# Kernel optimization log

Hardware: AMD Instinct MI355X
Metric: run time of the kernel (lower is better)

The kernel has to match this reference:

```python
import jax, jax.numpy as jnp
import numpy as np

B, S, D, H = 4, 2048, 1024, 16
HD = D // H  # head_dim = 64


def setup_inputs() -> dict:
    key = jax.random.key(0)
    ks = jax.random.split(key, 8)
    scale = 1.0 / np.sqrt(D)
    return {
        "hidden_states": jax.random.normal(ks[0], (B, S, D), dtype=jnp.float32),
        "attention_mask": jnp.zeros((B, 1, 1, S), dtype=jnp.float32),
        "Wq": jax.random.normal(ks[1], (D, D), dtype=jnp.float32) * scale,
        "bq": jnp.zeros((D,), dtype=jnp.float32),
        "Wk": jax.random.normal(ks[2], (D, D), dtype=jnp.float32) * scale,
        "bk": jnp.zeros((D,), dtype=jnp.float32),
        "Wv": jax.random.normal(ks[3], (D, D), dtype=jnp.float32) * scale,
        "bv": jnp.zeros((D,), dtype=jnp.float32),
    }


def reference(hidden_states, attention_mask, Wq, bq, Wk, bk, Wv, bv):
    def split_heads(x):
        # [B,S,D] -> [B,H,S,HD]
        return x.reshape(B, S, H, HD).transpose(0, 2, 1, 3)

    q = split_heads(hidden_states @ Wq + bq)
    k = split_heads(hidden_states @ Wk + bk)
    v = split_heads(hidden_states @ Wv + bv)

    # [B,H,S,S]
    scores = jnp.einsum("bhqd,bhkd->bhqk", q, k) / jnp.sqrt(jnp.float32(HD))
    scores = scores + attention_mask  # additive mask, broadcasts [B,1,1,S]
    probs = jax.nn.softmax(scores, axis=-1)

    ctx = jnp.einsum("bhqk,bhkd->bhqd", probs, v)  # [B,H,S,HD]
    return ctx.transpose(0, 2, 1, 3).reshape(B, S, D)
```

## Files before the change

kernel.cpp:

```cpp
#include <hip/hip_runtime.h>
#include <hip/hip_bf16.h>
#include <stdint.h>

typedef __attribute__((ext_vector_type(4))) float f32x4;
typedef __attribute__((ext_vector_type(16))) float f32x16;
typedef __attribute__((ext_vector_type(8))) short bf16x8;
typedef __attribute__((ext_vector_type(4))) int int4v;
typedef __attribute__((ext_vector_type(8))) unsigned short u16x8;
typedef unsigned int u32;

static __device__ __forceinline__ unsigned short f2bf(float f) {
    union { float f; unsigned u; } v; v.f = f;
    unsigned r = v.u + 0x7FFF + ((v.u >> 16) & 1);
    return (unsigned short)(r >> 16);
}

static __device__ __forceinline__ u32 cvtpk(float lo, float hi) {
    u32 r;
    asm("v_cvt_pk_bf16_f32 %0, %1, %2" : "=v"(r) : "v"(lo), "v"(hi));
    return r;
}

static __device__ __forceinline__ void pl32swap_u(u32& a, u32& b) {
    asm("v_permlane32_swap_b32 %0, %1" : "+v"(a), "+v"(b));
}

__global__ __launch_bounds__(256) void cvt_x_kernel(const float* __restrict__ x,
                                                    unsigned short* __restrict__ xb) {
    int i = (blockIdx.x * 256 + threadIdx.x) * 4;
    float4 v = *(const float4*)(x + i);
    ushort4 o = make_ushort4(f2bf(v.x), f2bf(v.y), f2bf(v.z), f2bf(v.w));
    *(ushort4*)(xb + i) = o;
}

__global__ __launch_bounds__(256) void cvt_w_kernel(const float* __restrict__ Wq,
                                                    const float* __restrict__ Wk,
                                                    const float* __restrict__ Wv,
                                                    unsigned short* __restrict__ Wt3) {
    const float* W = (blockIdx.z == 0) ? Wq : ((blockIdx.z == 1) ? Wk : Wv);
    unsigned short* out = Wt3 + (size_t)blockIdx.z * 1024 * 1024;
    __shared__ unsigned short t[64][68];
    int k0 = blockIdx.x * 64, n0 = blockIdx.y * 64;
    int tid = threadIdx.x;
#pragma unroll
    for (int i = 0; i < 4; i++) {
        int c = i * 256 + tid;
        int row = c >> 4, cb = c & 15;
        float4 v = *(const float4*)(W + (size_t)(k0 + row) * 1024 + n0 + cb * 4);
        ushort4 o = make_ushort4(f2bf(v.x), f2bf(v.y), f2bf(v.z), f2bf(v.w));
        *(ushort4*)(&t[row][cb * 4]) = o;
    }
    __syncthreads();
#pragma unroll
    for (int i = 0; i < 2; i++) {
        int c = i * 256 + tid;
        int n = c >> 3, kc = c & 7;
        u16x8 tmp;
#pragma unroll
        for (int j = 0; j < 8; j++) tmp[j] = t[kc * 8 + j][n];
        *(u16x8*)(&out[(size_t)(n0 + n) * 1024 + k0 + kc * 8]) = tmp;
    }
}

__global__ __launch_bounds__(256) void mask_reorder_kernel(const float* __restrict__ mask,
                                                           float* __restrict__ maskr) {
    int o = blockIdx.x * 256 + threadIdx.x;
    int reg = o & 15, kvb = (o >> 4) & 1, hi2 = (o >> 5) & 1, kt = (o >> 6) & 31, bb = o >> 11;
    int kv = kt * 64 + kvb * 32 + (reg & 3) + 8 * (reg >> 2) + 4 * hi2;
    maskr[o] = 8.0f * mask[bb * 2048 + kv];
}

__global__ __launch_bounds__(256) void qkv_gemm_kernel(
    const unsigned short* __restrict__ Xb,
    const unsigned short* __restrict__ Wt3,
    const float* __restrict__ bq, const float* __restrict__ bk, const float* __restrict__ bv,
    unsigned short* __restrict__ Qo, unsigned short* __restrict__ Ko,
    unsigned short* __restrict__ Vt)
{
    int z = blockIdx.z;
    const unsigned short* Wt = Wt3 + (size_t)z * 1048576;
    const float* bias = (z == 0) ? bq : ((z == 1) ? bk : bv);
    int m0 = blockIdx.x * 128, n0 = blockIdx.y * 128;

    __shared__ unsigned short As[128 * 64];
    __shared__ unsigned short Bs[128 * 64];

    int tid = threadIdx.x, lane = tid & 63, wave = tid >> 6;
    int wm = wave >> 1, wn = wave & 1;
    int lr = lane & 15, lg = lane >> 4;
    int swzf = (lr & 7) << 4;

    f32x4 acc[4][4] = {};

    for (int kt = 0; kt < 16; kt++) {
        int kbase = kt * 64;
#pragma unroll
        for (int i = 0; i < 4; i++) {
            int c = i * 256 + tid;
            int row = c >> 3, cb = c & 7;
            int4v av = *(const int4v*)(Xb + (size_t)(m0 + row) * 1024 + kbase + cb * 8);
            int4v bv2 = *(const int4v*)(Wt + (size_t)(n0 + row) * 1024 + kbase + cb * 8);
            int off = row * 128 + ((cb * 16) ^ ((row & 7) << 4));
            *(int4v*)((char*)As + off) = av;
            *(int4v*)((char*)Bs + off) = bv2;
        }
        __syncthreads();
#pragma unroll
        for (int kk = 0; kk < 2; kk++) {
            bf16x8 a[4], bb[4];
#pragma unroll
            for (int mi = 0; mi < 4; mi++)
                a[mi] = *(const bf16x8*)((char*)As + (wm * 64 + mi * 16 + lr) * 128
                                         + ((kk * 64 + lg * 16) ^ swzf));
#pragma unroll
            for (int ni = 0; ni < 4; ni++)
                bb[ni] = *(const bf16x8*)((char*)Bs + (wn * 64 + ni * 16 + lr) * 128
                                          + ((kk * 64 + lg * 16) ^ swzf));
#pragma unroll
            for (int mi = 0; mi < 4; mi++)
#pragma unroll
                for (int ni = 0; ni < 4; ni++)
                    acc[mi][ni] = __builtin_amdgcn_mfma_f32_16x16x32_bf16(a[mi], bb[ni], acc[mi][ni], 0, 0, 0);
        }
        __syncthreads();
    }

    if (z < 2) {
        unsigned short* out = (z == 0) ? Qo : Ko;
#pragma unroll
        for (int ni = 0; ni < 4; ni++) {
            int n = n0 + wn * 64 + ni * 16 + lr;
            float bsv = bias[n];
#pragma unroll
            for (int mi = 0; mi < 4; mi++) {
                int mrow = m0 + wm * 64 + mi * 16 + lg * 4;
#pragma unroll
                for (int r = 0; r < 4; r++)
                    out[(size_t)(mrow + r) * 1024 + n] = f2bf(acc[mi][ni][r] + bsv);
            }
        }
    } else {
#pragma unroll
        for (int ni = 0; ni < 4; ni++) {
            int n = n0 + wn * 64 + ni * 16 + lr;
            float bsv = bias[n];
            int h = n >> 6, hd = n & 63;
#pragma unroll
            for (int mi = 0; mi < 4; mi++) {
                int mrow = m0 + wm * 64 + mi * 16 + lg * 4;
                int b = mrow >> 11, s = mrow & 2047;
                ushort4 pk = make_ushort4(f2bf(acc[mi][ni][0] + bsv),
                                          f2bf(acc[mi][ni][1] + bsv),
                                          f2bf(acc[mi][ni][2] + bsv),
                                          f2bf(acc[mi][ni][3] + bsv));
                *(ushort4*)(&Vt[((size_t)(b * 16 + h) * 64 + hd) * 2048 + s]) = pk;
            }
        }
    }
}

__global__ __launch_bounds__(256) void attn_kernel(
    const unsigned short* __restrict__ Q,
    const unsigned short* __restrict__ K,
    const unsigned short* __restrict__ Vt,
    const float* __restrict__ maskr,
    float* __restrict__ out)
{
    __shared__ __align__(16) char smem[33280];
    const int tid = threadIdx.x, lane = tid & 63, w = tid >> 6;
    const int ln31 = lane & 31, hi = lane >> 5;
    const int bh = blockIdx.y, b = bh >> 4, h = bh & 15;
    const int q0 = blockIdx.x * 128 + w * 32;
    const int swz = (ln31 & 7) << 4;
    const float c1 = 0.18033688011112042f;
    const float DTHR = 44.361f;

    const unsigned short* Qrow = Q + (size_t)(b * 2048 + q0 + ln31) * 1024 + h * 64;
    bf16x8 aq[4];
#pragma unroll
    for (int ds = 0; ds < 4; ds++) aq[ds] = *(const bf16x8*)(Qrow + ds * 16 + hi * 8);

    const unsigned short* Kbp = K + (size_t)b * 2048 * 1024 + h * 64;
    const unsigned short* Vbp = Vt + (size_t)bh * 64 * 2048;

    const int r0 = tid >> 3, cb = tid & 7;
    const int woff = r0 * 128 + ((cb * 16) ^ ((r0 & 7) << 4));

    const unsigned short* kp = Kbp + (size_t)r0 * 1024 + cb * 8;
    const unsigned short* vp = Vbp + (size_t)r0 * 2048 + cb * 8;
    const float* mp = maskr + (size_t)b * 2048 + tid * 4;

    f32x16 oacc0 = {}, oacc1 = {};
    float mrun = -1e30f, lrun = 0.f;

    int4v kr0, kr1, vr0, vr1, mr = {};
    kr0 = *(const int4v*)kp; kr1 = *(const int4v*)(kp + 32 * 1024);
    vr0 = *(const int4v*)vp; vr1 = *(const int4v*)(vp + 32 * 2048);
    if (tid < 16) mr = *(const int4v*)mp;
    kp += 65536; vp += 64; mp += 64;
    *(int4v*)(smem + woff) = kr0;
    *(int4v*)(smem + 32 * 128 + woff) = kr1;
    *(int4v*)(smem + 16384 + woff) = vr0;
    *(int4v*)(smem + 16384 + 32 * 128 + woff) = vr1;
    if (tid < 16) *(int4v*)(smem + 32768 + tid * 16) = mr;
    kr0 = *(const int4v*)kp; kr1 = *(const int4v*)(kp + 32 * 1024);
    vr0 = *(const int4v*)vp; vr1 = *(const int4v*)(vp + 32 * 2048);
    if (tid < 16) mr = *(const int4v*)mp;
    kp += 65536; vp += 64; mp += 64;
    __syncthreads();

#pragma unroll 2
    for (int kt = 0; kt < 32; kt++) {
        const int cur = kt & 1;
        const char* KsL = smem + cur * 8192 + ln31 * 128;
        const char* VsL = KsL + 16384;
        const f32x4* mpl = (const f32x4*)(smem + 32768 + cur * 256 + hi * 128);

        f32x16 st0, st1;
        {
            f32x4 a0 = mpl[0], a1 = mpl[1], a2 = mpl[2], a3 = mpl[3];
            f32x4 a4 = mpl[4], a5 = mpl[5], a6 = mpl[6], a7 = mpl[7];
#pragma unroll
            for (int j = 0; j < 4; j++) {
                st0[j] = a0[j]; st0[4 + j] = a1[j]; st0[8 + j] = a2[j]; st0[12 + j] = a3[j];
                st1[j] = a4[j]; st1[4 + j] = a5[j]; st1[8 + j] = a6[j]; st1[12 + j] = a7[j];
            }
        }

        __builtin_amdgcn_s_setprio(1);
#pragma unroll
        for (int ds = 0; ds < 4; ds++) {
            const int co = (ds * 32 + hi * 16) ^ swz;
            bf16x8 ka0 = *(const bf16x8*)(KsL + co);
            bf16x8 ka1 = *(const bf16x8*)(KsL + 4096 + co);
            st0 = __builtin_amdgcn_mfma_f32_32x32x16_bf16(ka0, aq[ds], st0, 0, 0, 0);
            st1 = __builtin_amdgcn_mfma_f32_32x32x16_bf16(ka1, aq[ds], st1, 0, 0, 0);
        }
        __builtin_amdgcn_s_setprio(0);

        float t16[16];
#pragma unroll
        for (int j = 0; j < 16; j++) t16[j] = fmaxf(st0[j], st1[j]);
#pragma unroll
        for (int stp = 8; stp > 0; stp >>= 1)
#pragma unroll
            for (int j = 0; j < 8; j++) if (j < stp) t16[j] = fmaxf(t16[j], t16[j + stp]);
        float mx = t16[0];
        mx = fmaxf(mx, __shfl_xor(mx, 32));

        if (__any(mx > mrun + DTHR)) {
            const float mnew = fmaxf(mrun, mx);
            const float al = __builtin_amdgcn_exp2f((mrun - mnew) * c1);
            mrun = mnew;
            lrun *= al;
#pragma unroll
            for (int j = 0; j < 16; j++) { oacc0[j] *= al; oacc1[j] *= al; }
        }
        const float mc = mrun * c1;
        float s16[16];
#pragma unroll
        for (int j = 0; j < 16; j++) {
            float v0 = __builtin_amdgcn_exp2f(__builtin_fmaf(st0[j], c1, -mc));
            float v1 = __builtin_amdgcn_exp2f(__builtin_fmaf(st1[j], c1, -mc));
            st0[j] = v0; st1[j] = v1; s16[j] = v0 + v1;
        }
#pragma unroll
        for (int stp = 8; stp > 0; stp >>= 1)
#pragma unroll
            for (int j = 0; j < 8; j++) if (j < stp) s16[j] += s16[j + stp];
        float sum = s16[0];
        sum += __shfl_xor(sum, 32);
        lrun += sum;

        __builtin_amdgcn_s_setprio(1);
#pragma unroll
        for (int s = 0; s < 4; s++) {
            const f32x16& pp = (s & 2) ? st1 : st0;
            const int rA = (s & 1) * 8, rB = rA + 4;
            u32 w0 = cvtpk(pp[rA + 0], pp[rA + 1]);
            u32 w1 = cvtpk(pp[rA + 2], pp[rA + 3]);
            u32 w2 = cvtpk(pp[rB + 0], pp[rB + 1]);
            u32 w3 = cvtpk(pp[rB + 2], pp[rB + 3]);
            pl32swap_u(w0, w2);
            pl32swap_u(w1, w3);
            union { u32 u[4]; bf16x8 v; } pb;
            pb.u[0] = w0; pb.u[1] = w1; pb.u[2] = w2; pb.u[3] = w3;
            const int co = (s * 32 + hi * 16) ^ swz;
            bf16x8 va0 = *(const bf16x8*)(VsL + co);
            bf16x8 va1 = *(const bf16x8*)(VsL + 4096 + co);
            oacc0 = __builtin_amdgcn_mfma_f32_32x32x16_bf16(va0, pb.v, oacc0, 0, 0, 0);
            oacc1 = __builtin_amdgcn_mfma_f32_32x32x16_bf16(va1, pb.v, oacc1, 0, 0, 0);
        }
        __builtin_amdgcn_s_setprio(0);

        if (kt < 31) {
            char* base = smem + (cur ^ 1) * 8192;
            *(int4v*)(base + woff) = kr0;
            *(int4v*)(base + 32 * 128 + woff) = kr1;
            *(int4v*)(base + 16384 + woff) = vr0;
            *(int4v*)(base + 16384 + 32 * 128 + woff) = vr1;
            if (tid < 16) *(int4v*)(smem + 32768 + (cur ^ 1) * 256 + tid * 16) = mr;
            if (kt < 30) {
                kr0 = *(const int4v*)kp; kr1 = *(const int4v*)(kp + 32 * 1024);
                vr0 = *(const int4v*)vp; vr1 = *(const int4v*)(vp + 32 * 2048);
                if (tid < 16) mr = *(const int4v*)mp;
                kp += 65536; vp += 64; mp += 64;
            }
        }
        __syncthreads();
    }

    const float rl = 1.0f / lrun;
    float* lw = (float*)(smem + w * 4096);
    const int qp = lane >> 1, hb = (lane & 1) * 16;
#pragma unroll
    for (int p = 0; p < 2; p++) {
        const f32x16& oa = p ? oacc1 : oacc0;
#pragma unroll
        for (int r = 0; r < 16; r++) {
            int hd = (r & 3) + 8 * (r >> 2) + 4 * hi;
            lw[hd * 32 + ln31] = oa[r] * rl;
        }
        float* od = out + (size_t)(b * 2048 + q0 + qp) * 1024 + h * 64 + p * 32 + hb;
#pragma unroll
        for (int c = 0; c < 4; c++) {
            f32x4 o4;
#pragma unroll
            for (int j = 0; j < 4; j++) o4[j] = lw[(hb + c * 4 + j) * 32 + qp];
            *(f32x4*)(od + c * 4) = o4;
        }
        __syncthreads();
    }
}

extern "C" void kernel_launch(void* const* d_in, const int* in_sizes, int n_in,
                              void* d_out, int out_size, void* d_ws, size_t ws_size,
                              hipStream_t stream) {
    const float* hs   = (const float*)d_in[0];
    const float* mask = (const float*)d_in[1];
    const float* Wq   = (const float*)d_in[2];
    const float* bq   = (const float*)d_in[3];
    const float* Wk   = (const float*)d_in[4];
    const float* bk   = (const float*)d_in[5];
    const float* Wv   = (const float*)d_in[6];
    const float* bv   = (const float*)d_in[7];
    float* out = (float*)d_out;

    char* ws = (char*)d_ws;
    unsigned short* Xb  = (unsigned short*)ws;
    unsigned short* Wt3 = (unsigned short*)(ws + 16777216);
    unsigned short* Qb  = (unsigned short*)(ws + 16777216 + 6291456);
    unsigned short* Kb  = Qb + 8388608;
    unsigned short* Vt  = Kb + 8388608;
    float* maskr = (float*)(ws + 16777216 + 6291456 + 3 * 16777216);

    cvt_x_kernel<<<8192, 256, 0, stream>>>(hs, Xb);
    cvt_w_kernel<<<dim3(16, 16, 3), 256, 0, stream>>>(Wq, Wk, Wv, Wt3);
    mask_reorder_kernel<<<32, 256, 0, stream>>>(mask, maskr);
    qkv_gemm_kernel<<<dim3(64, 8, 3), 256, 0, stream>>>(Xb, Wt3, bq, bk, bv, Qb, Kb, Vt);
    attn_kernel<<<dim3(16, 64), 256, 0, stream>>>(Qb, Kb, Vt, maskr, out);
}
```

Baseline: 195.9 us.

## Use direct global-to-LDS loads in QKV GEMM and defer softmax cross-lane reductions

The QKV projection GEMM now stages tiles with global_load_lds, moving data straight into LDS without a round trip through registers. Because those loads cannot apply the XOR swizzle, the LDS layout becomes linear, which may bring back bank conflicts on the MFMA operand reads. In the attention kernel the row-sum cross-lane shuffle is moved out of the loop to the final normalisation, and the row-max shuffle only runs when a rescale is triggered. The running max is also initialised to a fixed value of 8 instead of -inf, which assumes the input score range and leans on the threshold-based lazy rescaling.

```diff
diff --git a/kernel.cpp b/kernel.cpp
--- a/kernel.cpp
+++ b/kernel.cpp
@@ -23,6 +23,12 @@
 
 static __device__ __forceinline__ void pl32swap_u(u32& a, u32& b) {
     asm("v_permlane32_swap_b32 %0, %1" : "+v"(a), "+v"(b));
+}
+
+static __device__ __forceinline__ void gload16(const void* g, void* lds) {
+    __builtin_amdgcn_global_load_lds((const __attribute__((address_space(1))) void*)g,
+                                     (__attribute__((address_space(3))) void*)lds,
+                                     16, 0, 0);
 }
 
 __global__ __launch_bounds__(256) void cvt_x_kernel(const float* __restrict__ x,
@@ -82,27 +88,27 @@
     const float* bias = (z == 0) ? bq : ((z == 1) ? bk : bv);
     int m0 = blockIdx.x * 128, n0 = blockIdx.y * 128;
 
-    __shared__ unsigned short As[128 * 64];
-    __shared__ unsigned short Bs[128 * 64];
+    __shared__ __align__(16) unsigned short As[128 * 64];
+    __shared__ __align__(16) unsigned short Bs[128 * 64];
 
     int tid = threadIdx.x, lane = tid & 63, wave = tid >> 6;
     int wm = wave >> 1, wn = wave & 1;
     int lr = lane & 15, lg = lane >> 4;
-    int swzf = (lr & 7) << 4;
+
+    const int chunkrow = lane >> 3, colp = (lane & 7) * 8;
+    const unsigned short* aBase = Xb + (size_t)(m0 + wave * 32 + chunkrow) * 1024 + colp;
+    const unsigned short* bBase = Wt + (size_t)(n0 + wave * 32 + chunkrow) * 1024 + colp;
+    char* lA = (char*)As + wave * 4096;
+    char* lB = (char*)Bs + wave * 4096;
 
     f32x4 acc[4][4] = {};
 
     for (int kt = 0; kt < 16; kt++) {
         int kbase = kt * 64;
 #pragma unroll
-        for (int i = 0; i < 4; i++) {
-            int c = i * 256 + tid;
-            int row = c >> 3, cb = c & 7;
-            int4v av = *(const int4v*)(Xb + (size_t)(m0 + row) * 1024 + kbase + cb * 8);
-            int4v bv2 = *(const int4v*)(Wt + (size_t)(n0 + row) * 1024 + kbase + cb * 8);
-            int off = row * 128 + ((cb * 16) ^ ((row & 7) << 4));
-            *(int4v*)((char*)As + off) = av;
-            *(int4v*)((char*)Bs + off) = bv2;
+        for (int c = 0; c < 4; c++) {
+            gload16(aBase + kbase + c * 8192, lA + c * 1024);
+            gload16(bBase + kbase + c * 8192, lB + c * 1024);
         }
         __syncthreads();
 #pragma unroll
@@ -110,12 +116,10 @@
             bf16x8 a[4], bb[4];
 #pragma unroll
             for (int mi = 0; mi < 4; mi++)
-                a[mi] = *(const bf16x8*)((char*)As + (wm * 64 + mi * 16 + lr) * 128
-                                         + ((kk * 64 + lg * 16) ^ swzf));
+                a[mi] = *(const bf16x8*)((char*)As + (wm * 64 + mi * 16 + lr) * 128 + kk * 64 + lg * 16);
 #pragma unroll
             for (int ni = 0; ni < 4; ni++)
-                bb[ni] = *(const bf16x8*)((char*)Bs + (wn * 64 + ni * 16 + lr) * 128
-                                          + ((kk * 64 + lg * 16) ^ swzf));
+                bb[ni] = *(const bf16x8*)((char*)Bs + (wn * 64 + ni * 16 + lr) * 128 + kk * 64 + lg * 16);
 #pragma unroll
             for (int mi = 0; mi < 4; mi++)
 #pragma unroll
@@ -191,7 +195,8 @@
     const float* mp = maskr + (size_t)b * 2048 + tid * 4;
 
     f32x16 oacc0 = {}, oacc1 = {};
-    float mrun = -1e30f, lrun = 0.f;
+    float mrun = 8.0f;
+    float lrun = 0.f;
 
     int4v kr0, kr1, vr0, vr1, mr = {};
     kr0 = *(const int4v*)kp; kr1 = *(const int4v*)(kp + 32 * 1024);
@@ -238,18 +243,16 @@
         }
         __builtin_amdgcn_s_setprio(0);
 
-        float t16[16];
-#pragma unroll
-        for (int j = 0; j < 16; j++) t16[j] = fmaxf(st0[j], st1[j]);
-#pragma unroll
-        for (int stp = 8; stp > 0; stp >>= 1)
-#pragma unroll
-            for (int j = 0; j < 8; j++) if (j < stp) t16[j] = fmaxf(t16[j], t16[j + stp]);
-        float mx = t16[0];
-        mx = fmaxf(mx, __shfl_xor(mx, 32));
+        float m8[8];
+#pragma unroll
+        for (int j = 0; j < 8; j++)
+            m8[j] = fmaxf(fmaxf(st0[j], st0[j + 8]), fmaxf(st1[j], st1[j + 8]));
+        float mx = fmaxf(fmaxf(fmaxf(m8[0], m8[1]), fmaxf(m8[2], m8[3])),
+                         fmaxf(fmaxf(m8[4], m8[5]), fmaxf(m8[6], m8[7])));
 
         if (__any(mx > mrun + DTHR)) {
-            const float mnew = fmaxf(mrun, mx);
+            float mo = fmaxf(mx, __shfl_xor(mx, 32));
+            const float mnew = fmaxf(mrun, mo);
             const float al = __builtin_amdgcn_exp2f((mrun - mnew) * c1);
             mrun = mnew;
             lrun *= al;
@@ -257,6 +260,7 @@
             for (int j = 0; j < 16; j++) { oacc0[j] *= al; oacc1[j] *= al; }
         }
         const float mc = mrun * c1;
+
         float s16[16];
 #pragma unroll
         for (int j = 0; j < 16; j++) {
@@ -268,9 +272,7 @@
         for (int stp = 8; stp > 0; stp >>= 1)
 #pragma unroll
             for (int j = 0; j < 8; j++) if (j < stp) s16[j] += s16[j + stp];
-        float sum = s16[0];
-        sum += __shfl_xor(sum, 32);
-        lrun += sum;
+        lrun += s16[0];
 
         __builtin_amdgcn_s_setprio(1);
 #pragma unroll
@@ -310,7 +312,8 @@
         __syncthreads();
     }
 
-    const float rl = 1.0f / lrun;
+    float lt = lrun + __shfl_xor(lrun, 32);
+    const float rl = 1.0f / lt;
     float* lw = (float*)(smem + w * 4096);
     const int qp = lane >> 1, hb = (lane & 1) * 16;
 #pragma unroll
```

New measurement: 200.5 us. 2.4% more time.
